# Optimization experiments

Hardware: AMD Instinct MI355X
Metric: run time of the kernel (lower is better)

## Reference

```python
import jax, jax.numpy as jnp
import numpy as np

EPS = 1e-06
SOUND_SPEED = 343.0
SUBBAND_EDGES = [500.0, 2000.0, 8000.0]
IS_SOUND_IDX = 0
RHO_IDX = 1
NUM_CANDIDATES = 64


def setup_inputs() -> dict:
    key = jax.random.key(0)
    ks = jax.random.split(key, 6)
    B, T, F, S, D = 16, 2048, 1025, 4, NUM_CANDIDATES
    phase = jax.random.normal(ks[0], (B, 1, T, F), dtype=jnp.float32)
    comb = jax.random.normal(ks[1], (B, 2, T, F), dtype=jnp.float32)
    scalar = jax.random.normal(ks[2], (B, T, S), dtype=jnp.float32)
    scalar_observed_mask = jax.random.uniform(ks[3], (B, T, S), dtype=jnp.float32)
    scalar_reliable_mask = jax.random.uniform(ks[4], (B, T, S), dtype=jnp.float32)
    stpacc = jax.random.normal(ks[5], (B, 1, T, D), dtype=jnp.float32)
    # STFT bin centers up to 24 kHz
    frequencies_hz = (jnp.arange(F, dtype=jnp.float32) * (24000.0 / (F - 1)))
    spacing_grid_hz = jnp.linspace(50.0, 1000.0, D, dtype=jnp.float32)
    return {
        'phase': phase, 'comb': comb, 'scalar': scalar,
        'scalar_observed_mask': scalar_observed_mask,
        'scalar_reliable_mask': scalar_reliable_mask,
        'stpacc': stpacc, 'frequencies_hz': frequencies_hz,
        'spacing_grid_hz': spacing_grid_hz,
    }


def _periodicity_basis(freq, spacing):
    # [D, F]: raised-cosine comb pattern for each candidate spacing
    pattern = 0.5 * (1.0 + jnp.cos(2.0 * np.pi * (freq[None, :] / jnp.maximum(spacing[:, None], 1e-06))))
    return pattern / jnp.maximum(pattern.mean(axis=-1, keepdims=True), EPS)


def _subband_masks(freq):
    # static boundaries: [min(f)] + edges + [max(f)+1]; all bands nonempty for this grid
    bounds = [jnp.min(freq)] + [jnp.float32(e) for e in SUBBAND_EDGES] + [jnp.max(freq) + 1.0]
    masks = [((freq >= lo) & (freq < hi)).astype(freq.dtype) for lo, hi in zip(bounds[:-1], bounds[1:])]
    return jnp.stack(masks, axis=0)  # [S_band, F]


def reference(phase, comb, scalar, scalar_observed_mask, scalar_reliable_mask,
              stpacc, frequencies_hz, spacing_grid_hz):
    freq = frequencies_hz.astype(phase.dtype)
    log_mag = phase[:, 0, :, :]                 # [B,T,F]
    smooth_d1 = comb[:, 0, :, :]
    abs_d1 = jnp.abs(comb[:, 1, :, :])
    log_mag_centered = log_mag - jnp.mean(log_mag, axis=-1, keepdims=True)
    trough = jax.nn.relu(-log_mag_centered)
    d1_strength = jax.nn.relu(abs_d1) + 0.25 * jax.nn.relu(jnp.abs(smooth_d1))
    trough = trough * (1.0 + d1_strength)
    trough = trough / jnp.maximum(jnp.mean(trough, axis=-1, keepdims=True), EPS)

    basis = _periodicity_basis(freq, spacing_grid_hz.astype(phase.dtype))  # [D,F]
    D, F = basis.shape
    periodic_score = jnp.einsum('btf,df->btd', trough, basis) / float(F)

    channels = [periodic_score]
    bands = _subband_masks(freq)                           # [Sb,F]
    denom = jnp.maximum(jnp.sum(bands, axis=-1), 1.0)      # [Sb]
    masked_basis = basis[None, :, :] * bands[:, None, :]   # [Sb,D,F]
    band_scores = jnp.einsum('btf,sdf->bstd', trough, masked_basis) / denom[None, :, None, None]
    channels += [band_scores[:, s] for s in range(bands.shape[0])]

    # stpacc projection (last dim already == D, no interpolation needed)
    stp = jax.nn.relu(stpacc[:, 0, :, :])
    stp = stp / jnp.maximum(jnp.mean(stp, axis=-1, keepdims=True), EPS)
    channels.append(stp)

    B, T = trough.shape[0], trough.shape[1]
    obs_quality = jnp.broadcast_to(jnp.mean(scalar_observed_mask, axis=-1, keepdims=True), (B, T, D))
    rel_quality = jnp.broadcast_to(jnp.mean(scalar_reliable_mask, axis=-1, keepdims=True), (B, T, D))
    channels.append(obs_quality)
    channels.append(rel_quality)

    is_sound = jnp.broadcast_to(jnp.clip(scalar[:, :, IS_SOUND_IDX:IS_SOUND_IDX + 1], 0.0, 1.0), (B, T, D))
    channels.append(is_sound)
    rho = jnp.broadcast_to(jnp.abs(jnp.clip(scalar[:, :, RHO_IDX:RHO_IDX + 1], -1.0, 1.0)), (B, T, D))
    channels.append(rho)

    raw_likelihood_seq = jnp.stack(channels, axis=-1)      # [B,T,D,10]
    raw_distance_logits_seq = jnp.mean(raw_likelihood_seq, axis=-1) * (0.5 + 0.5 * is_sound)

    distance_grid_cm = (100.0 * SOUND_SPEED) / (2.0 * jnp.maximum(spacing_grid_hz, 1e-06))
    return (raw_likelihood_seq, raw_distance_logits_seq,
            spacing_grid_hz.astype(phase.dtype), distance_grid_cm.astype(phase.dtype))
```

## Files before the change

kernel.cpp:

```cpp
#include <hip/hip_runtime.h>
#include <hip/hip_fp16.h>
#include <math.h>

#define Bn 16
#define Tn 2048
#define Fn 1025
#define KP 1056
#define KROW 1064
#define ROWS 16
#define Dn 64
#define EPSF 1e-6f

typedef __attribute__((ext_vector_type(8))) _Float16 f16x8;
typedef __attribute__((ext_vector_type(4))) _Float16 f16x4;
typedef __attribute__((ext_vector_type(4))) float f32x4;

__device__ inline float waveReduceSum(float v) {
#pragma unroll
  for (int off = 32; off > 0; off >>= 1) v += __shfl_xor(v, off, 64);
  return v;
}
__device__ inline void waveReduceSum2(float& a, float& b) {
#pragma unroll
  for (int off = 32; off > 0; off >>= 1) {
    a += __shfl_xor(a, off, 64);
    b += __shfl_xor(b, off, 64);
  }
}

__global__ __launch_bounds__(256) void prep_kernel(
    const float* __restrict__ freq, const float* __restrict__ spacing,
    _Float16* __restrict__ basisT, float* __restrict__ out2, float* __restrict__ out3) {
  __shared__ float wsum[4];
  const int d = blockIdx.x;
  const int tid = threadIdx.x;
  const float sp = fmaxf(spacing[d], 1e-6f);

  float pv[5];
  float lsum = 0.f;
#pragma unroll
  for (int it = 0; it < 5; ++it) {
    int f = tid + 256 * it;
    float p = 0.f;
    if (f < Fn) {
      double arg = 6.2831853071795864769 * (double)(freq[f] / sp);
      p = 0.5f * (1.0f + (float)cos(arg));
      lsum += p;
    }
    pv[it] = p;
  }
  float s = waveReduceSum(lsum);
  if ((tid & 63) == 0) wsum[tid >> 6] = s;
  __syncthreads();
  float inv = 1.0f / fmaxf((wsum[0] + wsum[1] + wsum[2] + wsum[3]) * (1.0f / 1025.0f), EPSF);

#pragma unroll
  for (int it = 0; it < 5; ++it) {
    int f = tid + 256 * it;
    if (f < KP) basisT[(size_t)d * KP + f] = (_Float16)(pv[it] * inv);
  }
  if (tid == 0) {
    out2[d] = spacing[d];
    out3[d] = 17150.0f / sp;
  }
}

__global__ __launch_bounds__(256, 3) void fused_kernel(
    const float* __restrict__ phase, const float* __restrict__ comb,
    const _Float16* __restrict__ basisT,
    const float* __restrict__ scalar, const float* __restrict__ obs_m,
    const float* __restrict__ rel_m, const float* __restrict__ stpacc,
    float* __restrict__ out0, float* __restrict__ out1) {
  __shared__ _Float16 uLDS[ROWS * KROW];
  __shared__ float rowScale[ROWS];

  const int lane = threadIdx.x & 63;
  const int w = __builtin_amdgcn_readfirstlane(threadIdx.x >> 6);
  const int row0 = blockIdx.x * ROWS;

  auto loadRow = [&](int row, float4* pv, float4* c0v, float4* c1v) {
    const int b = row >> 11;
    const int t = row & 2047;
    const float* prow  = phase + (size_t)row * Fn;
    const float* c0row = comb + ((size_t)(b * 2 + 0) * Tn + t) * Fn;
    const float* c1row = comb + ((size_t)(b * 2 + 1) * Tn + t) * Fn;
#pragma unroll
    for (int it = 0; it < 5; ++it) {
      const int i = lane + 64 * it;
      if (i < 256) {
        pv[it]  = *(const float4*)(prow  + 4 * i);
        c0v[it] = *(const float4*)(c0row + 4 * i);
        c1v[it] = *(const float4*)(c1row + 4 * i);
      } else if (i == 256) {
        pv[it]  = make_float4(prow[1024],  0.f, 0.f, 0.f);
        c0v[it] = make_float4(c0row[1024], 0.f, 0.f, 0.f);
        c1v[it] = make_float4(c1row[1024], 0.f, 0.f, 0.f);
      } else {
        pv[it]  = make_float4(0.f, 0.f, 0.f, 0.f);
        c0v[it] = make_float4(0.f, 0.f, 0.f, 0.f);
        c1v[it] = make_float4(0.f, 0.f, 0.f, 0.f);
      }
    }
  };
  auto rowSum = [&](const float4* pv) {
    float s = 0.f;
#pragma unroll
    for (int it = 0; it < 5; ++it)
      s += pv[it].x + pv[it].y + pv[it].z + pv[it].w;
    return s;
  };
  auto rowU = [&](int rl, float mean_lm, const float4* pv, const float4* c0v,
                  const float4* c1v) {
    _Float16* urow = uLDS + (size_t)rl * KROW;
    float su = 0.f;
#pragma unroll
    for (int it = 0; it < 5; ++it) {
      const int i = lane + 64 * it;
      float4 u;
      const float* pf = (const float*)&pv[it];
      const float* q0 = (const float*)&c0v[it];
      const float* q1 = (const float*)&c1v[it];
      float* uf = (float*)&u;
#pragma unroll
      for (int c2 = 0; c2 < 4; ++c2) {
        float tr = fmaxf(mean_lm - pf[c2], 0.f);
        float d1 = fabsf(q1[c2]) + 0.25f * fabsf(q0[c2]);
        uf[c2] = tr * (1.f + d1);
      }
      if (i > 256) { u.x = 0.f; u.y = 0.f; u.z = 0.f; u.w = 0.f; }
      else if (i == 256) { u.y = 0.f; u.z = 0.f; u.w = 0.f; }
      su += u.x + u.y + u.z + u.w;
      if (i < 264) {
        f16x4 hv;
#pragma unroll
        for (int c2 = 0; c2 < 4; ++c2) hv[c2] = (_Float16)uf[c2];
        *(f16x4*)(urow + 4 * i) = hv;
      }
    }
    return su;
  };

#pragma unroll 1
  for (int p = 0; p < 2; ++p) {
    const int rA = w * 4 + p * 2;
    const int rB = rA + 1;
    float4 pvA[5], c0A[5], c1A[5], pvB[5], c0B[5], c1B[5];
    loadRow(row0 + rA, pvA, c0A, c1A);
    loadRow(row0 + rB, pvB, c0B, c1B);
    float sA = rowSum(pvA), sB = rowSum(pvB);
    waveReduceSum2(sA, sB);
    float suA = rowU(rA, sA * (1.0f / 1025.0f), pvA, c0A, c1A);
    float suB = rowU(rB, sB * (1.0f / 1025.0f), pvB, c0B, c1B);
    waveReduceSum2(suA, suB);
    if (lane == 0) {
      rowScale[rA] = 1.0f / fmaxf(suA * (1.0f / 1025.0f), EPSF);
      rowScale[rB] = 1.0f / fmaxf(suB * (1.0f / 1025.0f), EPSF);
    }
  }
  __syncthreads();

  const int m16 = lane & 15;
  const int kg = lane >> 4;
  const int nh = w & 1;
  const int kh = w >> 1;
  const int d0 = nh * 32 + m16;

  const _Float16* ALp = uLDS + (size_t)m16 * KROW + kg * 8;
  const _Float16* B0 = basisT + (size_t)d0 * KP + kg * 8;
  const _Float16* B1 = basisT + (size_t)(d0 + 16) * KP + kg * 8;

  f32x4 acc0 = {0.f, 0.f, 0.f, 0.f};
  f32x4 acc1 = {0.f, 0.f, 0.f, 0.f};
  f32x4 s0a = acc0, s0b = acc0, s1a = acc0, s1b = acc0, s2a = acc0, s2b = acc0;

  auto loadA = [&](int kt) { return *(const f16x8*)(ALp + kt * 32); };
  auto tileA = [&](int kt, f16x8 a) {
    f16x8 b0 = *(const f16x8*)(B0 + kt * 32);
    f16x8 b1 = *(const f16x8*)(B1 + kt * 32);
    acc0 = __builtin_amdgcn_mfma_f32_16x16x32_f16(a, b0, acc0, 0, 0, 0);
    acc1 = __builtin_amdgcn_mfma_f32_16x16x32_f16(a, b1, acc1, 0, 0, 0);
  };
  auto boundary = [&](int kt, int KB, f32x4& sa, f32x4& sb) {
    f16x8 a = loadA(kt);
    const int kb = kt * 32 + kg * 8;
    f16x8 alo, ahi;
#pragma unroll
    for (int j = 0; j < 8; ++j) {
      bool lo = (kb + j) < KB;
      alo[j] = lo ? a[j] : (_Float16)0.f;
      ahi[j] = lo ? (_Float16)0.f : a[j];
    }
    tileA(kt, alo);
    sa = acc0; sb = acc1;
    tileA(kt, ahi);
  };

  if (kh == 0) {
    boundary(0, 22, s0a, s0b);
    tileA(1, loadA(1));
    boundary(2, 86, s1a, s1b);
#pragma unroll
    for (int kt = 3; kt < 10; ++kt) tileA(kt, loadA(kt));
    boundary(10, 342, s2a, s2b);
#pragma unroll
    for (int kt = 11; kt < 16; ++kt) tileA(kt, loadA(kt));
  } else {
#pragma unroll
    for (int kt = 16; kt < 33; ++kt) tileA(kt, loadA(kt));
  }
  __syncthreads();

  float* cumL = (float*)uLDS;
  auto stor = [&](int slot, const f32x4& v0, const f32x4& v1) {
#pragma unroll
    for (int r = 0; r < 4; ++r) {
      const int rr = kg * 4 + r;
      cumL[(rr * 5 + slot) * 65 + d0]      = v0[r];
      cumL[(rr * 5 + slot) * 65 + d0 + 16] = v1[r];
    }
  };
  if (kh == 0) {
    stor(0, s0a, s0b);
    stor(1, s1a, s1b);
    stor(2, s2a, s2b);
    stor(3, acc0, acc1);
  } else {
    stor(4, acc0, acc1);
  }
  __syncthreads();

#pragma unroll
  for (int k4 = 0; k4 < 4; ++k4) {
    const int rl = w * 4 + k4;
    const size_t bt = (size_t)(row0 + rl);
    const float rs = rowScale[rl];

    float sv = fmaxf(stpacc[bt * Dn + lane], 0.f);

    float q0 = cumL[(rl * 5 + 0) * 65 + lane];
    float q1 = cumL[(rl * 5 + 1) * 65 + lane];
    float q2 = cumL[(rl * 5 + 2) * 65 + lane];
    float q3 = cumL[(rl * 5 + 3) * 65 + lane] + cumL[(rl * 5 + 4) * 65 + lane];
    float b0 = q0, b1 = q1 - q0, b2 = q2 - q1, b3 = q3 - q2;

    float ssum = waveReduceSum(sv);
    float stp = sv / fmaxf(ssum * (1.0f / 64.0f), EPSF);

    float4 scv = *(const float4*)(scalar + bt * 4);
    float4 om  = *(const float4*)(obs_m  + bt * 4);
    float4 rm  = *(const float4*)(rel_m  + bt * 4);
    float obs_q = (om.x + om.y + om.z + om.w) * 0.25f;
    float rel_q = (rm.x + rm.y + rm.z + rm.w) * 0.25f;
    float is_snd = fminf(fmaxf(scv.x, 0.f), 1.f);
    float rho = fabsf(fminf(fmaxf(scv.y, -1.f), 1.f));

    float c0 = q3 * rs * (1.0f / 1025.0f);
    float c1 = b0 * rs * (1.0f / 22.0f);
    float c2 = b1 * rs * (1.0f / 64.0f);
    float c3 = b2 * rs * (1.0f / 256.0f);
    float c4 = b3 * rs * (1.0f / 683.0f);

    float mean10 = (c0 + c1 + c2 + c3 + c4 + stp + obs_q + rel_q + is_snd + rho) * 0.1f;
    float logit = mean10 * (0.5f + 0.5f * is_snd);

    float2* op = (float2*)(out0 + (bt * Dn + lane) * 10);
    op[0] = make_float2(c0, c1);
    op[1] = make_float2(c2, c3);
    op[2] = make_float2(c4, stp);
    op[3] = make_float2(obs_q, rel_q);
    op[4] = make_float2(is_snd, rho);
    out1[bt * Dn + lane] = logit;
  }
}

extern "C" void kernel_launch(void* const* d_in, const int* in_sizes, int n_in,
                              void* d_out, int out_size, void* d_ws, size_t ws_size,
                              hipStream_t stream) {
  const float* phase   = (const float*)d_in[0];
  const float* comb    = (const float*)d_in[1];
  const float* scalar  = (const float*)d_in[2];
  const float* obs_m   = (const float*)d_in[3];
  const float* rel_m   = (const float*)d_in[4];
  const float* stpacc  = (const float*)d_in[5];
  const float* freq    = (const float*)d_in[6];
  const float* spacing = (const float*)d_in[7];

  float* out  = (float*)d_out;
  float* out0 = out;
  float* out1 = out + (size_t)Bn * Tn * Dn * 10;
  float* out2 = out1 + (size_t)Bn * Tn * Dn;
  float* out3 = out2 + Dn;

  _Float16* basisT = (_Float16*)d_ws;

  prep_kernel<<<Dn, 256, 0, stream>>>(freq, spacing, basisT, out2, out3);
  fused_kernel<<<Bn * Tn / ROWS, 256, 0, stream>>>(
      phase, comb, basisT, scalar, obs_m, rel_m, stpacc, out0, out1);
}
```

Baseline: 124.0 us.

## Use dedicated LDS for cumulative sums, drop barrier, batch stpacc reductions

Adds a separate shared buffer for the per-row cumulative band sums so the epilogue no longer reuses the u tile, which removes one block-wide barrier after the MFMA loop. It also hoists the four stpacc loads ahead of the epilogue loop, batches their wave reductions into one interleaved shuffle sequence, and inserts scheduling barriers to keep the loads grouped. Occupancy hint is lowered from 3 to 2 blocks per SM, and the extra LDS (~20KB) raises shared memory per block.

```diff
diff --git a/kernel.cpp b/kernel.cpp
--- a/kernel.cpp
+++ b/kernel.cpp
@@ -27,6 +27,15 @@
     b += __shfl_xor(b, off, 64);
   }
 }
+__device__ inline void waveReduceSum4(float& a, float& b, float& c, float& d) {
+#pragma unroll
+  for (int off = 32; off > 0; off >>= 1) {
+    a += __shfl_xor(a, off, 64);
+    b += __shfl_xor(b, off, 64);
+    c += __shfl_xor(c, off, 64);
+    d += __shfl_xor(d, off, 64);
+  }
+}
 
 __global__ __launch_bounds__(256) void prep_kernel(
     const float* __restrict__ freq, const float* __restrict__ spacing,
@@ -65,13 +74,14 @@
   }
 }
 
-__global__ __launch_bounds__(256, 3) void fused_kernel(
+__global__ __launch_bounds__(256, 2) void fused_kernel(
     const float* __restrict__ phase, const float* __restrict__ comb,
     const _Float16* __restrict__ basisT,
     const float* __restrict__ scalar, const float* __restrict__ obs_m,
     const float* __restrict__ rel_m, const float* __restrict__ stpacc,
     float* __restrict__ out0, float* __restrict__ out1) {
   __shared__ _Float16 uLDS[ROWS * KROW];
+  __shared__ float cumS[ROWS * 5 * 65];
   __shared__ float rowScale[ROWS];
 
   const int lane = threadIdx.x & 63;
@@ -147,6 +157,7 @@
     float4 pvA[5], c0A[5], c1A[5], pvB[5], c0B[5], c1B[5];
     loadRow(row0 + rA, pvA, c0A, c1A);
     loadRow(row0 + rB, pvB, c0B, c1B);
+    __builtin_amdgcn_sched_barrier(0);
     float sA = rowSum(pvA), sB = rowSum(pvB);
     waveReduceSum2(sA, sB);
     float suA = rowU(rA, sA * (1.0f / 1025.0f), pvA, c0A, c1A);
@@ -208,15 +219,13 @@
 #pragma unroll
     for (int kt = 16; kt < 33; ++kt) tileA(kt, loadA(kt));
   }
-  __syncthreads();
-
-  float* cumL = (float*)uLDS;
+
   auto stor = [&](int slot, const f32x4& v0, const f32x4& v1) {
 #pragma unroll
     for (int r = 0; r < 4; ++r) {
       const int rr = kg * 4 + r;
-      cumL[(rr * 5 + slot) * 65 + d0]      = v0[r];
-      cumL[(rr * 5 + slot) * 65 + d0 + 16] = v1[r];
+      cumS[(rr * 5 + slot) * 65 + d0]      = v0[r];
+      cumS[(rr * 5 + slot) * 65 + d0 + 16] = v1[r];
     }
   };
   if (kh == 0) {
@@ -229,22 +238,29 @@
   }
   __syncthreads();
 
+  float sv[4];
+#pragma unroll
+  for (int k4 = 0; k4 < 4; ++k4)
+    sv[k4] = fmaxf(stpacc[(size_t)(row0 + w * 4 + k4) * Dn + lane], 0.f);
+  __builtin_amdgcn_sched_barrier(0);
+
+  float ss0 = sv[0], ss1 = sv[1], ss2 = sv[2], ss3 = sv[3];
+  waveReduceSum4(ss0, ss1, ss2, ss3);
+  float ssum[4] = {ss0, ss1, ss2, ss3};
+
 #pragma unroll
   for (int k4 = 0; k4 < 4; ++k4) {
     const int rl = w * 4 + k4;
     const size_t bt = (size_t)(row0 + rl);
     const float rs = rowScale[rl];
 
-    float sv = fmaxf(stpacc[bt * Dn + lane], 0.f);
-
-    float q0 = cumL[(rl * 5 + 0) * 65 + lane];
-    float q1 = cumL[(rl * 5 + 1) * 65 + lane];
-    float q2 = cumL[(rl * 5 + 2) * 65 + lane];
-    float q3 = cumL[(rl * 5 + 3) * 65 + lane] + cumL[(rl * 5 + 4) * 65 + lane];
+    float q0 = cumS[(rl * 5 + 0) * 65 + lane];
+    float q1 = cumS[(rl * 5 + 1) * 65 + lane];
+    float q2 = cumS[(rl * 5 + 2) * 65 + lane];
+    float q3 = cumS[(rl * 5 + 3) * 65 + lane] + cumS[(rl * 5 + 4) * 65 + lane];
     float b0 = q0, b1 = q1 - q0, b2 = q2 - q1, b3 = q3 - q2;
 
-    float ssum = waveReduceSum(sv);
-    float stp = sv / fmaxf(ssum * (1.0f / 64.0f), EPSF);
+    float stp = sv[k4] / fmaxf(ssum[k4] * (1.0f / 64.0f), EPSF);
 
     float4 scv = *(const float4*)(scalar + bt * 4);
     float4 om  = *(const float4*)(obs_m  + bt * 4);
```

New measurement: 126.0 us. No clear change (+1.6%).
